# Kernel tuning notes

Hardware: AMD Instinct MI355X
Metric: run time of the kernel (lower is better)

Reference implementation:

```python
import jax, jax.numpy as jnp
import numpy as np
import math

N_TF = 11
HID = 1024
DQK = HID // 4
LN_EPS = 1e-5


def coulomb_bias(screen_d, scale, n_tf):
    # distance matrix r[i,j] = |i-j|, shape [n_tf, n_tf]
    idx = jnp.arange(n_tf, dtype=jnp.float32)
    r = jnp.abs(idx[:, None] - idx[None, :])
    # V(r) = sum_k (-1)^k / sqrt(d_k^2 + r^2 + 1e-6)
    signs = jnp.array([(-1.0) ** k for k in range(screen_d.shape[0])], dtype=screen_d.dtype)
    denom = jnp.sqrt(screen_d[:, None, None] ** 2 + r[None, :, :] ** 2 + 1e-6)  # [K,n,n]
    w = jnp.sum(signs[:, None, None] / denom, axis=0)
    return w / (scale + 1e-6)


def setup_inputs() -> dict:
    key = jax.random.key(0)
    ks = jax.random.split(key, 8)
    s = 0.02
    return {
        "h": jax.random.normal(ks[0], (8192, N_TF, HID), jnp.float32),
        "Wq": jax.random.normal(ks[1], (DQK, HID), jnp.float32) * s,
        "bq": jnp.zeros((DQK,), jnp.float32),
        "Wk": jax.random.normal(ks[2], (DQK, HID), jnp.float32) * s,
        "bk": jnp.zeros((DQK,), jnp.float32),
        "Wv": jax.random.normal(ks[3], (HID, HID), jnp.float32) * s,
        "bv": jnp.zeros((HID,), jnp.float32),
        "Wo": jax.random.normal(ks[4], (HID, HID), jnp.float32) * s,
        "bo": jnp.zeros((HID,), jnp.float32),
        "gamma": jnp.ones((HID,), jnp.float32),
        "beta": jnp.zeros((HID,), jnp.float32),
        "screen_d": jnp.array([1.0, 3.0, 7.0], jnp.float32),
        "scale": jnp.array(1.0, jnp.float32),
    }


def reference(h, Wq, bq, Wk, bk, Wv, bv, Wo, bo, gamma, beta, screen_d, scale):
    # h: [B, T, H] stacked timeframe hidden states
    Q = jnp.einsum('bth,dh->btd', h, Wq) + bq  # [B,T,Dqk]
    K = jnp.einsum('bth,dh->btd', h, Wk) + bk
    V = jnp.einsum('bth,dh->btd', h, Wv) + bv  # [B,T,H]
    d_k = Q.shape[-1]
    scores = jnp.einsum('bqd,bkd->bqk', Q, K) / math.sqrt(d_k)  # [B,T,T]
    scores = scores + coulomb_bias(screen_d, scale, h.shape[1])[None, :, :]
    probs = jax.nn.softmax(scores, axis=-1)
    attended = jnp.einsum('bqk,bkh->bqh', probs, V)  # [B,T,H]
    out = jnp.einsum('bth,oh->bto', attended, Wo) + bo
    x = h + out
    mu = jnp.mean(x, axis=-1, keepdims=True)
    var = jnp.mean((x - mu) ** 2, axis=-1, keepdims=True)
    return (x - mu) * jax.lax.rsqrt(var + LN_EPS) * gamma + beta
```

## Files before the change

kernel.cpp:

```cpp
#include <hip/hip_runtime.h>
#include <cstdint>
#include <cstddef>

typedef _Float16 f16x8 __attribute__((ext_vector_type(8)));
typedef _Float16 f16x4 __attribute__((ext_vector_type(4)));
typedef float    f32x4 __attribute__((ext_vector_type(4)));

#define TFR  11
#define HID  1024
#define DQK  256
#define NBATCH 8192
#define MROWS (NBATCH*TFR)
#define NCAT 1536

#define OFF_QKHV ((size_t)0)
#define OFF_WCAT ((size_t)276824064)
#define OFF_WVT  ((size_t)279969792)
#define OFF_WO   ((size_t)282066944)
#define OFF_BCAT ((size_t)284164096)
#define OFF_BF   ((size_t)284170240)
#define OFF_TAB  ((size_t)284174336)

static __device__ __forceinline__ void gl2lds16(const void* g, void* l) {
  __builtin_amdgcn_global_load_lds(
      (const __attribute__((address_space(1))) void*)g,
      (__attribute__((address_space(3))) void*)l, 16, 0, 0);
}

__global__ __launch_bounds__(256)
void prep_w(const float* __restrict__ Wq, const float* __restrict__ Wk,
            const float* __restrict__ Wv, const float* __restrict__ Wo,
            const float* __restrict__ bq, const float* __restrict__ bk,
            const float* __restrict__ screen_d, const float* __restrict__ scale,
            _Float16* __restrict__ wcat, _Float16* __restrict__ wo16,
            _Float16* __restrict__ wvt, float* __restrict__ bcat,
            float* __restrict__ tab)
{
  const int idx = blockIdx.x * 256 + threadIdx.x;
  if (idx < 65536) {
    const int n = idx >> 7, c = (idx & 127) * 8;
    const float* src = (n < 256) ? &Wq[(size_t)n * 1024 + c]
                                 : &Wk[(size_t)(n - 256) * 1024 + c];
    f32x4 a = *(const f32x4*)src, b = *(const f32x4*)(src + 4);
    f16x8 o;
    o[0]=(_Float16)a[0]; o[1]=(_Float16)a[1]; o[2]=(_Float16)a[2]; o[3]=(_Float16)a[3];
    o[4]=(_Float16)b[0]; o[5]=(_Float16)b[1]; o[6]=(_Float16)b[2]; o[7]=(_Float16)b[3];
    *(f16x8*)&wcat[(size_t)n * 1024 + c] = o;
  } else if (idx < 196608) {
    const size_t e = (size_t)(idx - 65536) * 8;
    f32x4 a = *(const f32x4*)&Wo[e], b = *(const f32x4*)&Wo[e + 4];
    f16x8 o;
    o[0]=(_Float16)a[0]; o[1]=(_Float16)a[1]; o[2]=(_Float16)a[2]; o[3]=(_Float16)a[3];
    o[4]=(_Float16)b[0]; o[5]=(_Float16)b[1]; o[6]=(_Float16)b[2]; o[7]=(_Float16)b[3];
    *(f16x8*)&wo16[e] = o;
  } else if (idx < 327680) {
    const int j = idx - 196608;
    const int n = j & 1023, kc = j >> 10;
    f16x8 o;
#pragma unroll
    for (int e = 0; e < 8; ++e)
      o[e] = (_Float16)Wv[(size_t)(kc * 8 + e) * 1024 + n];
    *(f16x8*)&wvt[(size_t)n * 1024 + kc * 8] = o;
  }
  if (idx < NCAT)
    bcat[idx] = (idx < 256) ? bq[idx] : (idx < 512) ? bk[idx - 256] : 0.0f;
  if (idx < TFR * TFR) {
    const int i = idx / TFR, j = idx % TFR;
    const float r = fabsf((float)(i - j));
    float acc = 0.f, sign = 1.f;
    for (int k = 0; k < 3; ++k) {
      const float d = screen_d[k];
      acc += sign * rsqrtf(d * d + r * r + 1e-6f);
      sign = -sign;
    }
    tab[idx] = acc / (scale[0] + 1e-6f);
  }
}

__global__ __launch_bounds__(64)
void bfused_k(const float* __restrict__ Wo, const float* __restrict__ bv,
              const float* __restrict__ bo, float* __restrict__ bf)
{
  const int o = blockIdx.x, l = threadIdx.x;
  float acc = 0.f;
  for (int m = l; m < 1024; m += 64) acc += Wo[(size_t)o * 1024 + m] * bv[m];
#pragma unroll
  for (int off = 32; off >= 1; off >>= 1) acc += __shfl_xor(acc, off);
  if (l == 0) bf[o] = acc + bo[o];
}

struct __align__(16) GemmSmem {
  union {
    struct { _Float16 A[128 * 32]; _Float16 B[128 * 32]; } st;
    _Float16 E16[128 * 136];
  };
};

template <int AF32, int SWZ>
__global__ __launch_bounds__(256)
void gemm_f16(const void* __restrict__ Av, int lda,
              const _Float16* __restrict__ B,
              const float* __restrict__ bias,
              _Float16* __restrict__ out, int ldo, int K)
{
  __shared__ GemmSmem sm;
  const int t = threadIdx.x;
  int bx, by;
  if constexpr (SWZ) {
    const int orig = blockIdx.y * 12 + blockIdx.x;
    const int wg = (orig & 7) * 1056 + (orig >> 3);
    bx = wg % 12; by = wg / 12;
  } else {
    bx = blockIdx.x; by = blockIdx.y;
  }
  const int n0 = bx * 128;
  const int m0 = by * 128;
  const int w  = t >> 6, l = t & 63;
  const int wm = (w & 1) * 64, wn = (w >> 1) * 64;
  const int lr = l & 15, lg = l >> 4;

  f32x4 acc[4][4] = {};

  const int qa = t, qb = t + 256;
  _Float16* ldsA0 = &sm.st.A[qa * 8];
  _Float16* ldsA1 = &sm.st.A[qb * 8];
  _Float16* ldsB0 = &sm.st.B[qa * 8];
  _Float16* ldsB1 = &sm.st.B[qb * 8];
  const _Float16* Brow0 = B + (size_t)(n0 + (qa >> 2)) * K + (qa & 3) * 8;
  const _Float16* Brow1 = B + (size_t)(n0 + (qb >> 2)) * K + (qb & 3) * 8;
  const float*    A32r0 = (const float*)Av    + (size_t)(m0 + (qa >> 2)) * lda + (qa & 3) * 8;
  const float*    A32r1 = (const float*)Av    + (size_t)(m0 + (qb >> 2)) * lda + (qb & 3) * 8;
  const _Float16* A16r0 = (const _Float16*)Av + (size_t)(m0 + (qa >> 2)) * lda + (qa & 3) * 8;
  const _Float16* A16r1 = (const _Float16*)Av + (size_t)(m0 + (qb >> 2)) * lda + (qb & 3) * 8;

  for (int kt = 0; kt < K; kt += 32) {
    if constexpr (AF32) {
      gl2lds16(Brow0 + kt, ldsB0);
      gl2lds16(Brow1 + kt, ldsB1);
      f32x4 x0 = *(const f32x4*)(A32r0 + kt);
      f32x4 x1 = *(const f32x4*)(A32r0 + kt + 4);
      f32x4 y0 = *(const f32x4*)(A32r1 + kt);
      f32x4 y1 = *(const f32x4*)(A32r1 + kt + 4);
      f16x8 o0, o1;
#pragma unroll
      for (int e = 0; e < 4; ++e) {
        o0[e] = (_Float16)x0[e]; o0[4 + e] = (_Float16)x1[e];
        o1[e] = (_Float16)y0[e]; o1[4 + e] = (_Float16)y1[e];
      }
      *(f16x8*)ldsA0 = o0;
      *(f16x8*)ldsA1 = o1;
    } else {
      gl2lds16(A16r0 + kt, ldsA0);
      gl2lds16(A16r1 + kt, ldsA1);
      gl2lds16(Brow0 + kt, ldsB0);
      gl2lds16(Brow1 + kt, ldsB1);
    }
    __syncthreads();

    f16x8 af[4], bf[4];
#pragma unroll
    for (int mi = 0; mi < 4; ++mi)
      af[mi] = *(const f16x8*)&sm.st.A[(wm + mi * 16 + lr) * 32 + lg * 8];
#pragma unroll
    for (int ni = 0; ni < 4; ++ni)
      bf[ni] = *(const f16x8*)&sm.st.B[(wn + ni * 16 + lr) * 32 + lg * 8];
#pragma unroll
    for (int mi = 0; mi < 4; ++mi)
#pragma unroll
      for (int ni = 0; ni < 4; ++ni)
        acc[mi][ni] = __builtin_amdgcn_mfma_f32_16x16x32_f16(af[mi], bf[ni], acc[mi][ni], 0, 0, 0);
    __syncthreads();
  }

  float bias4[4];
#pragma unroll
  for (int ni = 0; ni < 4; ++ni)
    bias4[ni] = bias ? bias[n0 + wn + ni * 16 + lr] : 0.0f;
#pragma unroll
  for (int mi = 0; mi < 4; ++mi)
#pragma unroll
    for (int ni = 0; ni < 4; ++ni) {
      const int row = wm + mi * 16 + lg * 4;
      const int col = wn + ni * 16 + lr;
#pragma unroll
      for (int r = 0; r < 4; ++r)
        sm.E16[(row + r) * 136 + col] = (_Float16)(acc[mi][ni][r] + bias4[ni]);
    }
  __syncthreads();
#pragma unroll
  for (int i = 0; i < 8; ++i) {
    const int q = t + i * 256;
    const int row = q >> 4, c = (q & 15) * 8;
    *(f16x8*)&out[(size_t)(m0 + row) * ldo + n0 + c] = *(const f16x8*)&sm.E16[row * 136 + c];
  }
}

__global__ __launch_bounds__(256)
void fold_ln(const _Float16* __restrict__ qkhv, const float* __restrict__ h,
             const float* __restrict__ bfused, const float* __restrict__ tab,
             const float* __restrict__ gamma, const float* __restrict__ beta,
             float* __restrict__ out)
{
  __shared__ __align__(16) _Float16 sQH[TFR * NCAT];
  __shared__ float sSc[TFR][12];
  __shared__ float sP[TFR][12];
  __shared__ float sRed[TFR][8];
  const int t = threadIdx.x;
  const size_t qbase = (size_t)blockIdx.x * (TFR * NCAT);

  for (int q = t; q < TFR * NCAT / 8; q += 256)
    *(f16x8*)&sQH[q * 8] = *(const f16x8*)&qkhv[qbase + (size_t)q * 8];
  __syncthreads();

  if (t < TFR * TFR) {
    const int i = t / TFR, j = t % TFR;
    float acc = 0.f;
    for (int c = 0; c < DQK; c += 8) {
      f16x8 qv = *(const f16x8*)&sQH[i * NCAT + c];
      f16x8 kv = *(const f16x8*)&sQH[j * NCAT + DQK + c];
#pragma unroll
      for (int e = 0; e < 8; ++e) acc += (float)qv[e] * (float)kv[e];
    }
    sSc[i][j] = acc * 0.0625f + tab[t];
  }
  __syncthreads();

  if (t < TFR) {
    float mx = sSc[t][0];
    for (int j = 1; j < TFR; ++j) mx = fmaxf(mx, sSc[t][j]);
    float e[TFR], sum = 0.f;
    for (int j = 0; j < TFR; ++j) { e[j] = __expf(sSc[t][j] - mx); sum += e[j]; }
    const float inv = 1.f / sum;
    for (int j = 0; j < TFR; ++j) sP[t][j] = e[j] * inv;
  }
  __syncthreads();

  const int c = t * 4;
  const int w = t >> 6, l = t & 63;
  const f32x4 bfv = *(const f32x4*)&bfused[c];
  const size_t hbase = (size_t)blockIdx.x * (TFR * HID);
  f32x4 acc[TFR];
#pragma unroll
  for (int i = 0; i < TFR; ++i) {
    f32x4 a = {};
#pragma unroll
    for (int j = 0; j < TFR; ++j) {
      const float p = sP[i][j];
      const f16x4 hv = *(const f16x4*)&sQH[j * NCAT + 512 + c];
      a[0] += p * (float)hv[0]; a[1] += p * (float)hv[1];
      a[2] += p * (float)hv[2]; a[3] += p * (float)hv[3];
    }
    const f32x4 rv = *(const f32x4*)&h[hbase + (size_t)i * HID + c];
#pragma unroll
    for (int e = 0; e < 4; ++e) a[e] += bfv[e] + rv[e];
    acc[i] = a;
    float s  = a[0] + a[1] + a[2] + a[3];
    float s2 = a[0]*a[0] + a[1]*a[1] + a[2]*a[2] + a[3]*a[3];
#pragma unroll
    for (int off = 32; off >= 1; off >>= 1) {
      s  += __shfl_xor(s, off);
      s2 += __shfl_xor(s2, off);
    }
    if (l == 0) { sRed[i][w] = s; sRed[i][w + 4] = s2; }
  }
  __syncthreads();

  const f32x4 gv = *(const f32x4*)&gamma[c];
  const f32x4 bv = *(const f32x4*)&beta[c];
#pragma unroll
  for (int i = 0; i < TFR; ++i) {
    const float s  = sRed[i][0] + sRed[i][1] + sRed[i][2] + sRed[i][3];
    const float s2 = sRed[i][4] + sRed[i][5] + sRed[i][6] + sRed[i][7];
    const float mu  = s * (1.f / HID);
    const float var = s2 * (1.f / HID) - mu * mu;
    const float rs  = rsqrtf(var + 1e-5f);
    const f32x4 a = acc[i];
    f32x4 o;
#pragma unroll
    for (int e = 0; e < 4; ++e) o[e] = (a[e] - mu) * rs * gv[e] + bv[e];
    *(f32x4*)&out[hbase + (size_t)i * HID + c] = o;
  }
}

extern "C" void kernel_launch(void* const* d_in, const int* in_sizes, int n_in,
                              void* d_out, int out_size, void* d_ws, size_t ws_size,
                              hipStream_t stream)
{
  const float* h     = (const float*)d_in[0];
  const float* Wq    = (const float*)d_in[1];
  const float* bq    = (const float*)d_in[2];
  const float* Wk    = (const float*)d_in[3];
  const float* bk    = (const float*)d_in[4];
  const float* Wv    = (const float*)d_in[5];
  const float* bv    = (const float*)d_in[6];
  const float* Wo    = (const float*)d_in[7];
  const float* bo    = (const float*)d_in[8];
  const float* gamma = (const float*)d_in[9];
  const float* beta  = (const float*)d_in[10];
  const float* sd    = (const float*)d_in[11];
  const float* scal  = (const float*)d_in[12];
  float* out = (float*)d_out;

  char* w = (char*)d_ws;
  _Float16* qkhv = (_Float16*)(w + OFF_QKHV);
  _Float16* wcat = (_Float16*)(w + OFF_WCAT);
  _Float16* wvt  = (_Float16*)(w + OFF_WVT);
  _Float16* wo16 = (_Float16*)(w + OFF_WO);
  float* bcat    = (float*)(w + OFF_BCAT);
  float* bfused  = (float*)(w + OFF_BF);
  float* tab     = (float*)(w + OFF_TAB);

  prep_w<<<1280, 256, 0, stream>>>(Wq, Wk, Wv, Wo, bq, bk, sd, scal,
                                   wcat, wo16, wvt, bcat, tab);
  bfused_k<<<1024, 64, 0, stream>>>(Wo, bv, bo, bfused);

  gemm_f16<0, 0><<<dim3(8, 8), 256, 0, stream>>>(
      wo16, 1024, wvt, nullptr, wcat + (size_t)512 * 1024, 1024, 1024);

  gemm_f16<1, 1><<<dim3(12, 704), 256, 0, stream>>>(
      h, 1024, wcat, bcat, qkhv, NCAT, 1024);

  fold_ln<<<NBATCH, 256, 0, stream>>>(qkhv, h, bfused, tab, gamma, beta, out);
}
```

Baseline: 1.221 ms.

## Pre-convert h to fp16 and use a pipelined 256x256 GEMM

A separate pass now converts h to fp16, writing it into the output buffer as scratch. The main projection GEMM becomes a 512-thread 256x256-tile kernel that loads operands asynchronously straight into LDS, double-buffered, with explicit vmcnt waits, s_setprio around the MFMAs and a grouped tile order. fold_ln also loads the V rows and the h residual into registers early instead of staging all of QKHV in shared memory. This should raise MFMA utilisation and reuse per tile and overlap loads with compute, at the cost of an extra full read and write pass over h.

```diff
diff --git a/kernel.cpp b/kernel.cpp
--- a/kernel.cpp
+++ b/kernel.cpp
@@ -25,6 +25,18 @@
   __builtin_amdgcn_global_load_lds(
       (const __attribute__((address_space(1))) void*)g,
       (__attribute__((address_space(3))) void*)l, 16, 0, 0);
+}
+
+__global__ __launch_bounds__(256)
+void cvt_h(const float* __restrict__ h, _Float16* __restrict__ hf)
+{
+  const size_t i = ((size_t)blockIdx.x * 256 + threadIdx.x) * 8;
+  f32x4 a = *(const f32x4*)&h[i];
+  f32x4 b = *(const f32x4*)&h[i + 4];
+  f16x8 o;
+  o[0]=(_Float16)a[0]; o[1]=(_Float16)a[1]; o[2]=(_Float16)a[2]; o[3]=(_Float16)a[3];
+  o[4]=(_Float16)b[0]; o[5]=(_Float16)b[1]; o[6]=(_Float16)b[2]; o[7]=(_Float16)b[3];
+  *(f16x8*)&hf[i] = o;
 }
 
 __global__ __launch_bounds__(256)
@@ -96,25 +108,15 @@
   };
 };
 
-template <int AF32, int SWZ>
 __global__ __launch_bounds__(256)
-void gemm_f16(const void* __restrict__ Av, int lda,
-              const _Float16* __restrict__ B,
-              const float* __restrict__ bias,
-              _Float16* __restrict__ out, int ldo, int K)
+void gemm128(const _Float16* __restrict__ A, int lda,
+             const _Float16* __restrict__ B,
+             _Float16* __restrict__ out, int ldo, int K)
 {
   __shared__ GemmSmem sm;
-  const int t = threadIdx.x;
-  int bx, by;
-  if constexpr (SWZ) {
-    const int orig = blockIdx.y * 12 + blockIdx.x;
-    const int wg = (orig & 7) * 1056 + (orig >> 3);
-    bx = wg % 12; by = wg / 12;
-  } else {
-    bx = blockIdx.x; by = blockIdx.y;
-  }
-  const int n0 = bx * 128;
-  const int m0 = by * 128;
+  const int t  = threadIdx.x;
+  const int n0 = blockIdx.x * 128;
+  const int m0 = blockIdx.y * 128;
   const int w  = t >> 6, l = t & 63;
   const int wm = (w & 1) * 64, wn = (w >> 1) * 64;
   const int lr = l & 15, lg = l >> 4;
@@ -122,41 +124,21 @@
   f32x4 acc[4][4] = {};
 
   const int qa = t, qb = t + 256;
+  const _Float16* Arow0 = A + (size_t)(m0 + (qa >> 2)) * lda + (qa & 3) * 8;
+  const _Float16* Arow1 = A + (size_t)(m0 + (qb >> 2)) * lda + (qb & 3) * 8;
+  const _Float16* Brow0 = B + (size_t)(n0 + (qa >> 2)) * K + (qa & 3) * 8;
+  const _Float16* Brow1 = B + (size_t)(n0 + (qb >> 2)) * K + (qb & 3) * 8;
   _Float16* ldsA0 = &sm.st.A[qa * 8];
   _Float16* ldsA1 = &sm.st.A[qb * 8];
   _Float16* ldsB0 = &sm.st.B[qa * 8];
   _Float16* ldsB1 = &sm.st.B[qb * 8];
-  const _Float16* Brow0 = B + (size_t)(n0 + (qa >> 2)) * K + (qa & 3) * 8;
-  const _Float16* Brow1 = B + (size_t)(n0 + (qb >> 2)) * K + (qb & 3) * 8;
-  const float*    A32r0 = (const float*)Av    + (size_t)(m0 + (qa >> 2)) * lda + (qa & 3) * 8;
-  const float*    A32r1 = (const float*)Av    + (size_t)(m0 + (qb >> 2)) * lda + (qb & 3) * 8;
-  const _Float16* A16r0 = (const _Float16*)Av + (size_t)(m0 + (qa >> 2)) * lda + (qa & 3) * 8;
-  const _Float16* A16r1 = (const _Float16*)Av + (size_t)(m0 + (qb >> 2)) * lda + (qb & 3) * 8;
 
   for (int kt = 0; kt < K; kt += 32) {
-    if constexpr (AF32) {
-      gl2lds16(Brow0 + kt, ldsB0);
-      gl2lds16(Brow1 + kt, ldsB1);
-      f32x4 x0 = *(const f32x4*)(A32r0 + kt);
-      f32x4 x1 = *(const f32x4*)(A32r0 + kt + 4);
-      f32x4 y0 = *(const f32x4*)(A32r1 + kt);
-      f32x4 y1 = *(const f32x4*)(A32r1 + kt + 4);
-      f16x8 o0, o1;
-#pragma unroll
-      for (int e = 0; e < 4; ++e) {
-        o0[e] = (_Float16)x0[e]; o0[4 + e] = (_Float16)x1[e];
-        o1[e] = (_Float16)y0[e]; o1[4 + e] = (_Float16)y1[e];
-      }
-      *(f16x8*)ldsA0 = o0;
-      *(f16x8*)ldsA1 = o1;
-    } else {
-      gl2lds16(A16r0 + kt, ldsA0);
-      gl2lds16(A16r1 + kt, ldsA1);
-      gl2lds16(Brow0 + kt, ldsB0);
-      gl2lds16(Brow1 + kt, ldsB1);
-    }
+    gl2lds16(Arow0 + kt, ldsA0);
+    gl2lds16(Arow1 + kt, ldsA1);
+    gl2lds16(Brow0 + kt, ldsB0);
+    gl2lds16(Brow1 + kt, ldsB1);
     __syncthreads();
-
     f16x8 af[4], bf[4];
 #pragma unroll
     for (int mi = 0; mi < 4; ++mi)
@@ -172,10 +154,6 @@
     __syncthreads();
   }
 
-  float bias4[4];
-#pragma unroll
-  for (int ni = 0; ni < 4; ++ni)
-    bias4[ni] = bias ? bias[n0 + wn + ni * 16 + lr] : 0.0f;
 #pragma unroll
   for (int mi = 0; mi < 4; ++mi)
 #pragma unroll
@@ -184,7 +162,7 @@
       const int col = wn + ni * 16 + lr;
 #pragma unroll
       for (int r = 0; r < 4; ++r)
-        sm.E16[(row + r) * 136 + col] = (_Float16)(acc[mi][ni][r] + bias4[ni]);
+        sm.E16[(row + r) * 136 + col] = (_Float16)acc[mi][ni][r];
     }
   __syncthreads();
 #pragma unroll
@@ -192,6 +170,109 @@
     const int q = t + i * 256;
     const int row = q >> 4, c = (q & 15) * 8;
     *(f16x8*)&out[(size_t)(m0 + row) * ldo + n0 + c] = *(const f16x8*)&sm.E16[row * 136 + c];
+  }
+}
+
+#define STAGE256(h) do {                                                     \
+    const int kt2_ = (h) >> 2, isB_ = (h) & 1, ks2_ = ((h) >> 1) & 1;        \
+    const int gcol_ = kt2_ * 64 + ks2_ * 32;                                 \
+    _Float16* d_ = sm.S + (kt2_ & 1) * 32768 + isB_ * 16384 + ks2_ * 8192    \
+                   + t * 8;                                                  \
+    const _Float16* s1_ = (isB_ ? Bp1 : Ap1) + gcol_;                        \
+    const _Float16* s2_ = (isB_ ? Bp2 : Ap2) + gcol_;                        \
+    gl2lds16(s1_, d_);                                                       \
+    gl2lds16(s2_, d_ + 4096);                                                \
+  } while (0)
+
+#define PHASE256(g, VM, ISSUE) do {                                          \
+    asm volatile("s_waitcnt vmcnt(" #VM ")" ::: "memory");                   \
+    __builtin_amdgcn_s_barrier();                                            \
+    const int ks_ = (g) & 1, buf_ = ((g) >> 1) & 1;                          \
+    const int ab_ = buf_ * 32768 + ks_ * 8192;                               \
+    f16x8 af_[8], bf_[4];                                                    \
+    _Pragma("unroll")                                                        \
+    for (int mi = 0; mi < 8; ++mi)                                           \
+      af_[mi] = *(const f16x8*)&sm.S[ab_ + (wr*128 + mi*16 + lr)*32 + lg*8]; \
+    _Pragma("unroll")                                                        \
+    for (int ni = 0; ni < 4; ++ni)                                           \
+      bf_[ni] = *(const f16x8*)&sm.S[ab_ + 16384 + (wc*64 + ni*16 + lr)*32   \
+                                     + lg*8];                                \
+    if (ISSUE) { STAGE256(2*(g)+6); STAGE256(2*(g)+7); }                     \
+    __builtin_amdgcn_s_setprio(1);                                           \
+    _Pragma("unroll")                                                        \
+    for (int mi = 0; mi < 8; ++mi)                                           \
+      _Pragma("unroll")                                                      \
+      for (int ni = 0; ni < 4; ++ni)                                         \
+        acc[mi][ni] = __builtin_amdgcn_mfma_f32_16x16x32_f16(                \
+            af_[mi], bf_[ni], acc[mi][ni], 0, 0, 0);                         \
+    __builtin_amdgcn_s_setprio(0);                                           \
+  } while (0)
+
+__global__ __launch_bounds__(512, 2)
+void gemm256(const _Float16* __restrict__ A,
+             const _Float16* __restrict__ B,
+             const float* __restrict__ bias,
+             _Float16* __restrict__ out)
+{
+  __shared__ union {
+    _Float16 S[65536];
+    _Float16 E[128 * 264];
+  } sm;
+  const int t = threadIdx.x;
+  const int orig = blockIdx.y * 6 + blockIdx.x;
+  const int wg = (orig & 7) * 264 + (orig >> 3);
+  const int bx = wg % 6, by = wg / 6;
+  const int n0 = bx * 256, m0 = by * 256;
+
+  const int w  = t >> 6, l = t & 63;
+  const int wr = w >> 2, wc = w & 3;
+  const int lr = l & 15, lg = l >> 4;
+
+  const int srow = t >> 2, cA = (t & 3) * 8;
+  const _Float16* Ap1 = A + (size_t)(m0 + srow) * 1024 + cA;
+  const _Float16* Ap2 = Ap1 + (size_t)128 * 1024;
+  const _Float16* Bp1 = B + (size_t)(n0 + srow) * 1024 + cA;
+  const _Float16* Bp2 = Bp1 + (size_t)128 * 1024;
+
+  f32x4 acc[8][4] = {};
+
+  STAGE256(0); STAGE256(1); STAGE256(2); STAGE256(3); STAGE256(4); STAGE256(5);
+
+  for (int g = 0; g < 29; ++g) { PHASE256(g, 8, 1); }
+  PHASE256(29, 8, 0);
+  PHASE256(30, 4, 0);
+  PHASE256(31, 0, 0);
+
+  __syncthreads();
+
+  float bias4[4];
+#pragma unroll
+  for (int ni = 0; ni < 4; ++ni)
+    bias4[ni] = bias[n0 + wc * 64 + ni * 16 + lr];
+
+#pragma unroll
+  for (int p = 0; p < 2; ++p) {
+    if (wr == p) {
+#pragma unroll
+      for (int mi = 0; mi < 8; ++mi)
+#pragma unroll
+        for (int ni = 0; ni < 4; ++ni) {
+          const int row = mi * 16 + lg * 4;
+          const int col = wc * 64 + ni * 16 + lr;
+#pragma unroll
+          for (int r = 0; r < 4; ++r)
+            sm.E[(row + r) * 264 + col] = (_Float16)(acc[mi][ni][r] + bias4[ni]);
+        }
+    }
+    __syncthreads();
+#pragma unroll
+    for (int i = 0; i < 8; ++i) {
+      const int q = t + i * 512;
+      const int row = q >> 5, c = (q & 31) * 8;
+      *(f16x8*)&out[(size_t)(m0 + p * 128 + row) * NCAT + n0 + c] =
+          *(const f16x8*)&sm.E[row * 264 + c];
+    }
+    __syncthreads();
   }
 }
 
@@ -201,23 +282,36 @@
              const float* __restrict__ gamma, const float* __restrict__ beta,
              float* __restrict__ out)
 {
-  __shared__ __align__(16) _Float16 sQH[TFR * NCAT];
+  __shared__ __align__(16) _Float16 sQK[TFR * 512];
   __shared__ float sSc[TFR][12];
   __shared__ float sP[TFR][12];
   __shared__ float sRed[TFR][8];
   const int t = threadIdx.x;
   const size_t qbase = (size_t)blockIdx.x * (TFR * NCAT);
-
-  for (int q = t; q < TFR * NCAT / 8; q += 256)
-    *(f16x8*)&sQH[q * 8] = *(const f16x8*)&qkhv[qbase + (size_t)q * 8];
+  const size_t hbase = (size_t)blockIdx.x * (TFR * HID);
+  const int c = t * 4;
+
+  f16x4 hvj[TFR];
+  f32x4 hres[TFR];
+#pragma unroll
+  for (int j = 0; j < TFR; ++j)
+    hvj[j] = *(const f16x4*)&qkhv[qbase + (size_t)j * NCAT + 512 + c];
+#pragma unroll
+  for (int j = 0; j < TFR; ++j)
+    hres[j] = *(const f32x4*)&h[hbase + (size_t)j * HID + c];
+
+  for (int q = t; q < TFR * 512 / 8; q += 256) {
+    const int row = q >> 6, ch = q & 63;
+    *(f16x8*)&sQK[q * 8] = *(const f16x8*)&qkhv[qbase + (size_t)row * NCAT + ch * 8];
+  }
   __syncthreads();
 
   if (t < TFR * TFR) {
     const int i = t / TFR, j = t % TFR;
     float acc = 0.f;
-    for (int c = 0; c < DQK; c += 8) {
-      f16x8 qv = *(const f16x8*)&sQH[i * NCAT + c];
-      f16x8 kv = *(const f16x8*)&sQH[j * NCAT + DQK + c];
+    for (int cc = 0; cc < DQK; cc += 8) {
+      f16x8 qv = *(const f16x8*)&sQK[i * 512 + cc];
+      f16x8 kv = *(const f16x8*)&sQK[j * 512 + 256 + cc];
 #pragma unroll
       for (int e = 0; e < 8; ++e) acc += (float)qv[e] * (float)kv[e];
     }
@@ -235,10 +329,8 @@
   }
   __syncthreads();
 
-  const int c = t * 4;
   const int w = t >> 6, l = t & 63;
   const f32x4 bfv = *(const f32x4*)&bfused[c];
-  const size_t hbase = (size_t)blockIdx.x * (TFR * HID);
   f32x4 acc[TFR];
 #pragma unroll
   for (int i = 0; i < TFR; ++i) {
@@ -246,13 +338,11 @@
 #pragma unroll
     for (int j = 0; j < TFR; ++j) {
       const float p = sP[i][j];
-      const f16x4 hv = *(const f16x4*)&sQH[j * NCAT + 512 + c];
-      a[0] += p * (float)hv[0]; a[1] += p * (float)hv[1];
-      a[2] += p * (float)hv[2]; a[3] += p * (float)hv[3];
-    }
-    const f32x4 rv = *(const f32x4*)&h[hbase + (size_t)i * HID + c];
-#pragma unroll
-    for (int e = 0; e < 4; ++e) a[e] += bfv[e] + rv[e];
+      a[0] += p * (float)hvj[j][0]; a[1] += p * (float)hvj[j][1];
+      a[2] += p * (float)hvj[j][2]; a[3] += p * (float)hvj[j][3];
+    }
+#pragma unroll
+    for (int e = 0; e < 4; ++e) a[e] += bfv[e] + hres[i][e];
     acc[i] = a;
     float s  = a[0] + a[1] + a[2] + a[3];
     float s2 = a[0]*a[0] + a[1]*a[1] + a[2]*a[2] + a[3]*a[3];
@@ -310,15 +400,17 @@
   float* bfused  = (float*)(w + OFF_BF);
   float* tab     = (float*)(w + OFF_TAB);
 
+  _Float16* hcvt = (_Float16*)d_out;
+
+  cvt_h<<<45056, 256, 0, stream>>>(h, hcvt);
   prep_w<<<1280, 256, 0, stream>>>(Wq, Wk, Wv, Wo, bq, bk, sd, scal,
                                    wcat, wo16, wvt, bcat, tab);
   bfused_k<<<1024, 64, 0, stream>>>(Wo, bv, bo, bfused);
 
-  gemm_f16<0, 0><<<dim3(8, 8), 256, 0, stream>>>(
-      wo16, 1024, wvt, nullptr, wcat + (size_t)512 * 1024, 1024, 1024);
-
-  gemm_f16<1, 1><<<dim3(12, 704), 256, 0, stream>>>(
-      h, 1024, wcat, bcat, qkhv, NCAT, 1024);
+  gemm128<<<dim3(8, 8), 256, 0, stream>>>(
+      wo16, 1024, wvt, wcat + (size_t)512 * 1024, 1024, 1024);
+
+  gemm256<<<dim3(6, 352), 512, 0, stream>>>(hcvt, wcat, bcat, qkhv);
 
   fold_ln<<<NBATCH, 256, 0, stream>>>(qkhv, h, bfused, tab, gamma, beta, out);
 }
```

Result: faster. 1.100 ms (-10.0%).
